# Optimization experiments

Hardware: AMD Instinct MI355X
Metric: run time of the kernel (lower is better)

Reference implementation:

```python
import jax, jax.numpy as jnp
import numpy as np
import math

B, S, D, H, FF = 32, 577, 768, 12, 3072
Dh = D // H
EPS = 1e-5


def layer_norm(x, w, b):
    mu = jnp.mean(x, axis=-1, keepdims=True)
    var = jnp.mean(jnp.square(x - mu), axis=-1, keepdims=True)
    return (x - mu) * jax.lax.rsqrt(var + EPS) * w + b


def setup_inputs() -> dict:
    key = jax.random.key(0)
    ks = jax.random.split(key, 12)
    s = 0.02
    return {
        "x": jax.random.normal(ks[0], (B, S, D), dtype=jnp.float32),
        "ln1_w": jnp.ones((D,), jnp.float32),
        "ln1_b": jnp.zeros((D,), jnp.float32),
        # stacked per-head Q/K/V projections (head order matches torch concat order)
        "Wq": jax.random.normal(ks[1], (H, D, Dh), jnp.float32) * s,
        "bq": jnp.zeros((H, Dh), jnp.float32),
        "Wk": jax.random.normal(ks[2], (H, D, Dh), jnp.float32) * s,
        "bk": jnp.zeros((H, Dh), jnp.float32),
        "Wv": jax.random.normal(ks[3], (H, D, Dh), jnp.float32) * s,
        "bv": jnp.zeros((H, Dh), jnp.float32),
        "Wo": jax.random.normal(ks[4], (D, D), jnp.float32) * s,
        "bo": jnp.zeros((D,), jnp.float32),
        "ln2_w": jnp.ones((D,), jnp.float32),
        "ln2_b": jnp.zeros((D,), jnp.float32),
        "W1": jax.random.normal(ks[5], (D, FF), jnp.float32) * s,
        "b1": jnp.zeros((FF,), jnp.float32),
        "W2": jax.random.normal(ks[6], (FF, D), jnp.float32) * s,
        "b2": jnp.zeros((D,), jnp.float32),
    }


def reference(x, ln1_w, ln1_b, Wq, bq, Wk, bk, Wv, bv, Wo, bo, ln2_w, ln2_b, W1, b1, W2, b2):
    # pre-norm attention
    h = layer_norm(x, ln1_w, ln1_b)  # [B,S,D]
    q = jnp.einsum('bsd,hde->bhse', h, Wq) + bq[:, None, :]
    k = jnp.einsum('bsd,hde->bhse', h, Wk) + bk[:, None, :]
    v = jnp.einsum('bsd,hde->bhse', h, Wv) + bv[:, None, :]
    scores = jnp.einsum('bhse,bhte->bhst', q, k) / math.sqrt(Dh)
    probs = jax.nn.softmax(scores, axis=-1)
    ctx = jnp.einsum('bhst,bhte->bhse', probs, v)  # [B,H,S,Dh]
    ctx = ctx.transpose(0, 2, 1, 3).reshape(B, S, H * Dh)  # concat heads
    attn_out = ctx @ Wo + bo
    x = x + attn_out
    # pre-norm MLP (exact GELU, as nn.GELU default)
    h2 = layer_norm(x, ln2_w, ln2_b)
    mlp = jax.nn.gelu(h2 @ W1 + b1, approximate=False) @ W2 + b2
    return x + mlp
```

## Files before the change

kernel.cpp:

```cpp
#include <hip/hip_runtime.h>
#include <hip/hip_bf16.h>
#include <stdint.h>

#define B_ 32
#define S_ 577
#define D_ 768
#define H_ 12
#define FF_ 3072
#define MROWS (B_*S_)

typedef __attribute__((ext_vector_type(8))) short sh8;
typedef __attribute__((ext_vector_type(4))) float f32x4;
typedef __attribute__((ext_vector_type(4))) unsigned short us4;

static __device__ __forceinline__ unsigned short f2b(float f) {
  __hip_bfloat16 h = __float2bfloat16(f);
  return *reinterpret_cast<unsigned short*>(&h);
}
static __device__ __forceinline__ float b2f(unsigned short u) {
  __hip_bfloat16 h;
  *reinterpret_cast<unsigned short*>(&h) = u;
  return __bfloat162float(h);
}

static __device__ __forceinline__ float fast_gelu(float v) {
  const float z = fabsf(v) * 0.70710678118f;
  const float t = __builtin_amdgcn_rcpf(__builtin_fmaf(0.3275911f, z, 1.0f));
  float p = 1.061405429f;
  p = __builtin_fmaf(p, t, -1.453152027f);
  p = __builtin_fmaf(p, t,  1.421413741f);
  p = __builtin_fmaf(p, t, -0.284496736f);
  p = __builtin_fmaf(p, t,  0.254829592f);
  p = p * t;
  const float e = __expf(-z * z);
  const float erf_abs = __builtin_fmaf(-p, e, 1.0f);
  const float erf_v = copysignf(erf_abs, v);
  const float hv = 0.5f * v;
  return __builtin_fmaf(hv, erf_v, hv);
}

#define GLOAD_LDS16(gp, lp) \
  __builtin_amdgcn_global_load_lds((const __attribute__((address_space(1))) unsigned int*)(gp), \
                                   (__attribute__((address_space(3))) unsigned int*)(lp), 16, 0, 0)

static __device__ __forceinline__ void packT_body(
    const float* __restrict__ src, unsigned short* __restrict__ dst,
    int K, int N, int kb, int nb, float scl, int tid)
{
  __shared__ unsigned short t[64][65];
  const int c = tid & 63, r4 = tid >> 6;
#pragma unroll
  for (int p = 0; p < 16; ++p) {
    const int ko = p * 4 + r4;
    t[c][ko] = f2b(src[(size_t)(kb + ko) * N + nb + c] * scl);
  }
  __syncthreads();
#pragma unroll
  for (int p = 0; p < 16; ++p) {
    const int rr = p * 4 + r4;
    dst[(size_t)(nb + rr) * K + kb + c] = t[rr][c];
  }
}

__global__ __launch_bounds__(256) void pack_all(
    const float* __restrict__ Wq, const float* __restrict__ Wk,
    const float* __restrict__ Wv, const float* __restrict__ Wo,
    const float* __restrict__ W1, const float* __restrict__ W2,
    const float* __restrict__ bq, const float* __restrict__ bk,
    const float* __restrict__ bv,
    unsigned short* __restrict__ wqkvT, unsigned short* __restrict__ woT,
    unsigned short* __restrict__ w1T, unsigned short* __restrict__ w2T,
    float* __restrict__ biasq)
{
  const int b = blockIdx.x;
  const int tid = threadIdx.x;
  if (b < 144) {
    packT_body(Wo, woT, 768, 768, (b / 12) * 64, (b % 12) * 64, 1.f, tid);
  } else if (b < 720) {
    const int i = b - 144;
    packT_body(W1, w1T, 768, 3072, (i / 48) * 64, (i % 48) * 64, 1.f, tid);
  } else if (b < 1296) {
    const int i = b - 720;
    packT_body(W2, w2T, 3072, 768, (i / 12) * 64, (i % 12) * 64, 1.f, tid);
  } else if (b < 1728) {
    const int i = b - 1296;
    const int kb = i % 12, h = (i / 12) % 12, which = i / 144;
    const float* src = ((which == 0) ? Wq : (which == 1) ? Wk : Wv) + (size_t)h * 768 * 64;
    unsigned short* db = wqkvT + (size_t)(which * 768 + h * 64) * 768;
    packT_body(src, db, 768, 64, kb * 64, 0, which == 0 ? 0.125f : 1.f, tid);
  } else {
    const int idx = (b - 1728) * 256 + tid;
    if (idx < 2304) {
      const int wb = idx / 768, rb = idx - wb * 768;
      const float* bb = (wb == 0) ? bq : (wb == 1) ? bk : bv;
      biasq[idx] = bb[rb] * (wb == 0 ? 0.125f : 1.f);
    }
  }
}

__global__ __launch_bounds__(192) void ln_bf16(
    const float* __restrict__ x, const float* __restrict__ w, const float* __restrict__ bse,
    unsigned short* __restrict__ out)
{
  const int row = blockIdx.x;
  const int tid = threadIdx.x;
  const float* xr = x + (size_t)row * 768;
  const f32x4 v = *(const f32x4*)(xr + tid * 4);
  float s  = v[0] + v[1] + v[2] + v[3];
  float ss = v[0]*v[0] + v[1]*v[1] + v[2]*v[2] + v[3]*v[3];
#pragma unroll
  for (int off = 32; off >= 1; off >>= 1) {
    s  += __shfl_xor(s, off);
    ss += __shfl_xor(ss, off);
  }
  __shared__ float red[6];
  const int wv = tid >> 6, ln = tid & 63;
  if (ln == 0) { red[wv] = s; red[wv + 3] = ss; }
  __syncthreads();
  s  = red[0] + red[1] + red[2];
  ss = red[3] + red[4] + red[5];
  const float mu = s * (1.f / 768.f);
  const float var = ss * (1.f / 768.f) - mu * mu;
  const float rs = rsqrtf(var + 1e-5f);
  const f32x4 w4 = *(const f32x4*)(w + tid * 4);
  const f32x4 b4 = *(const f32x4*)(bse + tid * 4);
  us4 o;
#pragma unroll
  for (int e = 0; e < 4; ++e) o[e] = f2b((v[e] - mu) * rs * w4[e] + b4[e]);
  *(us4*)(out + (size_t)row * 768 + tid * 4) = o;
}

template<int EPI>
__global__ __launch_bounds__(256, 4) void gemm128(
    const unsigned short* __restrict__ A, const unsigned short* __restrict__ Bt,
    const float* __restrict__ bias, const float* __restrict__ res,
    unsigned short* __restrict__ obf, float* __restrict__ of32,
    int M, int N, int K)
{
  __shared__ __align__(16) unsigned short sAB[2][128 * 64];
  const int tid = threadIdx.x;
  const int wid = tid >> 6, ln = tid & 63;
  const int wr = wid >> 1, wc = wid & 1;
  const int l15 = ln & 15, lg = ln >> 4;
  const int l7 = l15 & 7;
  const int uo0 = ((lg) ^ l7) * 8;
  const int uo1 = ((4 + lg) ^ l7) * 8;
  const int srow = ln >> 3;
  const int scol = ((ln & 7) ^ srow) * 8;
  const int NT = K >> 6;

  const int gx = N >> 7;
  const int gm = (M + 127) >> 7;
  const int nwg = gridDim.x;
  const int q = nwg >> 3, r = nwg & 7;
  const int x = blockIdx.x & 7, ii = blockIdx.x >> 3;
  const int wg = (x < r ? x * (q + 1) : r * (q + 1) + (x - r) * q) + ii;
  int bm, bn;
  {
    const int g8 = gx >> 3, rem = gx & 7;
    const int per_full = gm << 3;
    if (wg < g8 * per_full) {
      const int bg = wg / per_full;
      const int r2 = wg - bg * per_full;
      bm = r2 >> 3; bn = (bg << 3) + (r2 & 7);
    } else {
      const int r2 = wg - g8 * per_full;
      bm = r2 / rem; bn = (g8 << 3) + (r2 - bm * rem);
    }
  }

  const int arow = wr * 64 + l15;
  const int brow = wc * 64 + l15;

  const unsigned short* ap[4];
  const unsigned short* bp[4];
#pragma unroll
  for (int j = 0; j < 4; ++j) {
    int ga = bm * 128 + (wid * 4 + j) * 8 + srow; if (ga >= M) ga = M - 1;
    ap[j] = A + (size_t)ga * K + scol;
    const int gb = bn * 128 + (wid * 4 + j) * 8 + srow;
    bp[j] = Bt + (size_t)gb * K + scol;
  }
  unsigned short* const lA = sAB[0] + wid * 4 * 512;
  unsigned short* const lB = sAB[1] + wid * 4 * 512;

  f32x4 acc[4][4] = {};

  for (int t = 0; t < NT; ++t) {
    __syncthreads();
#pragma unroll
    for (int j = 0; j < 4; ++j) { GLOAD_LDS16(ap[j], lA + j * 512); ap[j] += 64; }
#pragma unroll
    for (int j = 0; j < 4; ++j) { GLOAD_LDS16(bp[j], lB + j * 512); bp[j] += 64; }
    asm volatile("s_waitcnt vmcnt(0)" ::: "memory");
    __syncthreads();

#pragma unroll
    for (int kk = 0; kk < 2; ++kk) {
      const int uo = kk ? uo1 : uo0;
      sh8 af[4], bf[4];
#pragma unroll
      for (int mi = 0; mi < 4; ++mi)
        af[mi] = *(const sh8*)(sAB[0] + (arow + mi * 16) * 64 + uo);
#pragma unroll
      for (int ni = 0; ni < 4; ++ni)
        bf[ni] = *(const sh8*)(sAB[1] + (brow + ni * 16) * 64 + uo);
#pragma unroll
      for (int mi = 0; mi < 4; ++mi)
#pragma unroll
        for (int ni = 0; ni < 4; ++ni)
          acc[mi][ni] = __builtin_amdgcn_mfma_f32_16x16x32_bf16(af[mi], bf[ni], acc[mi][ni], 0, 0, 0);
    }
  }

  constexpr int ESTR = 132;
  float* eps = (float*)sAB;
  const int ecol = (tid & 31) * 4;
  const int gcol = bn * 128 + ecol;
  const f32x4 bvh = *(const f32x4*)(bias + gcol);
  const int erow0 = tid >> 5;
#pragma unroll
  for (int pass = 0; pass < 4; ++pass) {
    __syncthreads();
    if (wr == (pass >> 1)) {
      const int mib = (pass & 1) * 2;
#pragma unroll
      for (int ml = 0; ml < 2; ++ml)
#pragma unroll
        for (int ni = 0; ni < 4; ++ni)
#pragma unroll
          for (int rr = 0; rr < 4; ++rr)
            eps[(ml * 16 + lg * 4 + rr) * ESTR + wc * 64 + ni * 16 + l15] = acc[mib + ml][ni][rr];
    }
    __syncthreads();
#pragma unroll
    for (int pp = 0; pp < 4; ++pp) {
      const int rl = pp * 8 + erow0;
      const int grow = bm * 128 + pass * 32 + rl;
      if (grow < M) {
        f32x4 v = *(const f32x4*)(eps + rl * ESTR + ecol);
        v += bvh;
        if (EPI == 2) {
#pragma unroll
          for (int e = 0; e < 4; ++e) v[e] = fast_gelu(v[e]);
        }
        if (EPI == 1) {
          const f32x4 rv = *(const f32x4*)(res + (size_t)grow * N + gcol);
          v += rv;
          *(f32x4*)(of32 + (size_t)grow * N + gcol) = v;
        } else {
          us4 o = { f2b(v[0]), f2b(v[1]), f2b(v[2]), f2b(v[3]) };
          *(us4*)(obf + (size_t)grow * N + gcol) = o;
        }
      }
    }
  }
}

__global__ __launch_bounds__(512) void attn(
    const unsigned short* __restrict__ qkv, unsigned short* __restrict__ ctx)
{
  constexpr int KP = 72;
  __shared__ __align__(16) unsigned short sQ[128 * KP];
  __shared__ __align__(16) unsigned short sK[64 * KP];
  __shared__ __align__(16) unsigned short sVT[64 * KP];
  __shared__ __align__(16) unsigned short sP[8][16 * KP];
  const int tid = threadIdx.x, wv = tid >> 6, ln = tid & 63;
  const int l15 = ln & 15, lg = ln >> 4;
  const int b = blockIdx.z, h = blockIdx.y, qt = blockIdx.x;
  const size_t base = (size_t)b * S_ * 2304 + h * 64;
  const unsigned short* qp = qkv + base;
  const unsigned short* kp = qkv + base + 768;
  const unsigned short* vp = qkv + base + 1536;

  {
    const int r = tid >> 2, c = (tid & 3) * 16;
    int row = qt * 128 + r; if (row >= S_) row = S_ - 1;
    const unsigned short* g = qp + (size_t)row * 2304 + c;
    *(sh8*)(sQ + r * KP + c)     = *(const sh8*)g;
    *(sh8*)(sQ + r * KP + c + 8) = *(const sh8*)(g + 8);
  }

  const int kr = tid >> 3, kc = (tid & 7) * 8;
  const unsigned short* krow = kp + (size_t)kr * 2304 + kc;
  unsigned short* const sKdst = sK + kr * KP + kc;
  const int ve = tid & 63, vkvb = tid >> 6;
  const unsigned short* vrow = vp + (size_t)vkvb * 8 * 2304 + ve;
  unsigned short* const sVdst = sVT + ve * KP + vkvb * 8;

  f32x4 oacc[4] = {};
  float m_run = -1e30f, l_run = 0.f;
  const int nt = (S_ + 63) / 64;
  for (int t = 0; t < nt; ++t) {
    __syncthreads();
    if (t < nt - 1) {
      *(sh8*)sKdst = *(const sh8*)krow;
      krow += (size_t)64 * 2304;
      {
        unsigned short val[8];
#pragma unroll
        for (int j = 0; j < 8; ++j) val[j] = vrow[(size_t)j * 2304];
        *(sh8*)sVdst = *(sh8*)val;
        vrow += (size_t)64 * 2304;
      }
    } else {
      {
        int row = t * 64 + kr; if (row >= S_) row = S_ - 1;
        *(sh8*)sKdst = *(const sh8*)(kp + (size_t)row * 2304 + kc);
      }
      {
        unsigned short val[8];
#pragma unroll
        for (int j = 0; j < 8; ++j) {
          int row = t * 64 + vkvb * 8 + j; if (row >= S_) row = S_ - 1;
          val[j] = vp[(size_t)row * 2304 + ve];
        }
        *(sh8*)sVdst = *(sh8*)val;
      }
    }
    __syncthreads();

    f32x4 sacc[4] = {};
#pragma unroll
    for (int kk = 0; kk < 2; ++kk) {
      sh8 bq = *(const sh8*)(sQ + (wv * 16 + l15) * KP + kk * 32 + lg * 8);
#pragma unroll
      for (int f = 0; f < 4; ++f) {
        sh8 ak = *(const sh8*)(sK + (f * 16 + l15) * KP + kk * 32 + lg * 8);
        sacc[f] = __builtin_amdgcn_mfma_f32_16x16x32_bf16(ak, bq, sacc[f], 0, 0, 0);
      }
    }

    if (t == nt - 1) {
#pragma unroll
      for (int f = 0; f < 4; ++f)
#pragma unroll
        for (int r = 0; r < 4; ++r)
          if (t * 64 + f * 16 + lg * 4 + r >= S_) sacc[f][r] = -1e30f;
    }
    float pmax = -1e30f;
#pragma unroll
    for (int f = 0; f < 4; ++f)
#pragma unroll
      for (int r = 0; r < 4; ++r) pmax = fmaxf(pmax, sacc[f][r]);
    pmax = fmaxf(pmax, __shfl_xor(pmax, 16));
    pmax = fmaxf(pmax, __shfl_xor(pmax, 32));
    const float mnew = fmaxf(m_run, pmax);
    const float alpha = __expf(m_run - mnew);
    float psum = 0.f;
    unsigned short pb[4][4];
#pragma unroll
    for (int f = 0; f < 4; ++f)
#pragma unroll
      for (int r = 0; r < 4; ++r) {
        const float p = __expf(sacc[f][r] - mnew);
        psum += p;
        pb[f][r] = f2b(p);
      }
    psum += __shfl_xor(psum, 16);
    psum += __shfl_xor(psum, 32);
    l_run = l_run * alpha + psum;
    m_run = mnew;
#pragma unroll
    for (int f = 0; f < 4; ++f) {
      oacc[f][0] *= alpha; oacc[f][1] *= alpha;
      oacc[f][2] *= alpha; oacc[f][3] *= alpha;
    }
#pragma unroll
    for (int f = 0; f < 4; ++f) {
      us4 pk = { pb[f][0], pb[f][1], pb[f][2], pb[f][3] };
      *(us4*)(sP[wv] + l15 * KP + f * 16 + lg * 4) = pk;
    }
    __syncthreads();

#pragma unroll
    for (int kk = 0; kk < 2; ++kk) {
      sh8 bp = *(const sh8*)(sP[wv] + l15 * KP + kk * 32 + lg * 8);
#pragma unroll
      for (int fe = 0; fe < 4; ++fe) {
        sh8 av = *(const sh8*)(sVT + (fe * 16 + l15) * KP + kk * 32 + lg * 8);
        oacc[fe] = __builtin_amdgcn_mfma_f32_16x16x32_bf16(av, bp, oacc[fe], 0, 0, 0);
      }
    }
  }

  const int qa = qt * 128 + wv * 16 + l15;
  if (qa < S_) {
    const float inv = 1.f / l_run;
    const size_t orow = ((size_t)b * S_ + qa) * 768 + h * 64;
#pragma unroll
    for (int fe = 0; fe < 4; ++fe) {
      unsigned short pk[4];
#pragma unroll
      for (int r = 0; r < 4; ++r) pk[r] = f2b(oacc[fe][r] * inv);
      *(us4*)(ctx + orow + fe * 16 + lg * 4) = *(us4*)pk;
    }
  }
}

extern "C" void kernel_launch(void* const* d_in, const int* in_sizes, int n_in,
                              void* d_out, int out_size, void* d_ws, size_t ws_size,
                              hipStream_t stream)
{
  const float* x    = (const float*)d_in[0];
  const float* ln1w = (const float*)d_in[1];
  const float* ln1b = (const float*)d_in[2];
  const float* Wq   = (const float*)d_in[3];
  const float* bq   = (const float*)d_in[4];
  const float* Wk   = (const float*)d_in[5];
  const float* bk   = (const float*)d_in[6];
  const float* Wv   = (const float*)d_in[7];
  const float* bv   = (const float*)d_in[8];
  const float* Wo   = (const float*)d_in[9];
  const float* bo   = (const float*)d_in[10];
  const float* ln2w = (const float*)d_in[11];
  const float* ln2b = (const float*)d_in[12];
  const float* W1   = (const float*)d_in[13];
  const float* b1   = (const float*)d_in[14];
  const float* W2   = (const float*)d_in[15];
  const float* b2   = (const float*)d_in[16];
  float* out = (float*)d_out;
  char* ws = (char*)d_ws;

  unsigned short* wqkvT = (unsigned short*)(ws + 0);
  unsigned short* woT   = (unsigned short*)(ws + 3538944);
  unsigned short* w1T   = (unsigned short*)(ws + 4718592);
  unsigned short* w2T   = (unsigned short*)(ws + 9437184);
  float*          biasq = (float*)(ws + 14155776);
  unsigned short* hbf   = (unsigned short*)(ws + 14164992);
  unsigned short* qkvb  = (unsigned short*)(ws + 42525696);
  unsigned short* ctxb  = (unsigned short*)(ws + 127607808);
  unsigned short* mlp1  = qkvb;

  pack_all<<<1737, 256, 0, stream>>>(Wq, Wk, Wv, Wo, W1, W2, bq, bk, bv,
                                     wqkvT, woT, w1T, w2T, biasq);

  ln_bf16<<<MROWS, 192, 0, stream>>>(x, ln1w, ln1b, hbf);
  gemm128<0><<<145 * 18, 256, 0, stream>>>(hbf, wqkvT, biasq, nullptr, qkvb, nullptr,
                                           MROWS, 2304, 768);
  attn<<<dim3(5, 12, 32), 512, 0, stream>>>(qkvb, ctxb);
  gemm128<1><<<145 * 6, 256, 0, stream>>>(ctxb, woT, bo, x, nullptr, out,
                                          MROWS, 768, 768);
  ln_bf16<<<MROWS, 192, 0, stream>>>(out, ln2w, ln2b, hbf);
  gemm128<2><<<145 * 24, 256, 0, stream>>>(hbf, w1T, b1, nullptr, mlp1, nullptr,
                                           MROWS, 3072, 768);
  gemm128<1><<<145 * 6, 256, 0, stream>>>(mlp1, w2T, b2, out, nullptr, out,
                                          MROWS, 768, 3072);
}
```

Before: 464.5 us.

## Fuse LN1 into pack kernel and register-prefetch K/V tiles in attention

Merges the first LayerNorm into the weight-packing launch as extra blocks, removing one kernel launch and letting the two independent jobs overlap. In the attention kernel, the next K/V tile is loaded into registers while the current tile is being computed, so global-load latency is hidden behind the MFMA work. The barrier between writing P to shared memory and the PV MFMA is removed, since each wave only reads its own sP slice. Register prefetch raises register pressure, and the merged kernel now holds two unlike kinds of work, which may hurt occupancy.

```diff
diff --git a/kernel.cpp b/kernel.cpp
--- a/kernel.cpp
+++ b/kernel.cpp
@@ -62,7 +62,43 @@
   }
 }
 
-__global__ __launch_bounds__(256) void pack_all(
+static __device__ __forceinline__ void ln_body256(
+    const float* __restrict__ x, const float* __restrict__ w,
+    const float* __restrict__ bse, unsigned short* __restrict__ out,
+    int row, int tid)
+{
+  __shared__ float red[6];
+  const int wv = tid >> 6, ln = tid & 63;
+  f32x4 v = {};
+  float s = 0.f, ss = 0.f;
+  if (tid < 192) {
+    v = *(const f32x4*)(x + (size_t)row * 768 + tid * 4);
+    s  = v[0] + v[1] + v[2] + v[3];
+    ss = v[0]*v[0] + v[1]*v[1] + v[2]*v[2] + v[3]*v[3];
+  }
+#pragma unroll
+  for (int off = 32; off >= 1; off >>= 1) {
+    s  += __shfl_xor(s, off);
+    ss += __shfl_xor(ss, off);
+  }
+  if (ln == 0 && wv < 3) { red[wv] = s; red[wv + 3] = ss; }
+  __syncthreads();
+  if (tid < 192) {
+    s  = red[0] + red[1] + red[2];
+    ss = red[3] + red[4] + red[5];
+    const float mu = s * (1.f / 768.f);
+    const float var = ss * (1.f / 768.f) - mu * mu;
+    const float rs = rsqrtf(var + 1e-5f);
+    const f32x4 w4 = *(const f32x4*)(w + tid * 4);
+    const f32x4 b4 = *(const f32x4*)(bse + tid * 4);
+    us4 o;
+#pragma unroll
+    for (int e = 0; e < 4; ++e) o[e] = f2b((v[e] - mu) * rs * w4[e] + b4[e]);
+    *(us4*)(out + (size_t)row * 768 + tid * 4) = o;
+  }
+}
+
+__global__ __launch_bounds__(256) void pack_ln(
     const float* __restrict__ Wq, const float* __restrict__ Wk,
     const float* __restrict__ Wv, const float* __restrict__ Wo,
     const float* __restrict__ W1, const float* __restrict__ W2,
@@ -70,7 +106,9 @@
     const float* __restrict__ bv,
     unsigned short* __restrict__ wqkvT, unsigned short* __restrict__ woT,
     unsigned short* __restrict__ w1T, unsigned short* __restrict__ w2T,
-    float* __restrict__ biasq)
+    float* __restrict__ biasq,
+    const float* __restrict__ x, const float* __restrict__ ln1w,
+    const float* __restrict__ ln1b, unsigned short* __restrict__ hbf)
 {
   const int b = blockIdx.x;
   const int tid = threadIdx.x;
@@ -88,13 +126,15 @@
     const float* src = ((which == 0) ? Wq : (which == 1) ? Wk : Wv) + (size_t)h * 768 * 64;
     unsigned short* db = wqkvT + (size_t)(which * 768 + h * 64) * 768;
     packT_body(src, db, 768, 64, kb * 64, 0, which == 0 ? 0.125f : 1.f, tid);
-  } else {
+  } else if (b < 1737) {
     const int idx = (b - 1728) * 256 + tid;
     if (idx < 2304) {
       const int wb = idx / 768, rb = idx - wb * 768;
       const float* bb = (wb == 0) ? bq : (wb == 1) ? bk : bv;
       biasq[idx] = bb[rb] * (wb == 0 ? 0.125f : 1.f);
     }
+  } else {
+    ln_body256(x, ln1w, ln1b, hbf, b - 1737, tid);
   }
 }
 
@@ -288,37 +328,39 @@
   const unsigned short* vrow = vp + (size_t)vkvb * 8 * 2304 + ve;
   unsigned short* const sVdst = sVT + ve * KP + vkvb * 8;
 
+  const int nt = (S_ + 63) / 64;
+  sh8 kreg = *(const sh8*)krow;
+  unsigned short vreg[8];
+#pragma unroll
+  for (int j = 0; j < 8; ++j) vreg[j] = vrow[(size_t)j * 2304];
+  krow += (size_t)64 * 2304;
+  vrow += (size_t)64 * 2304;
+
   f32x4 oacc[4] = {};
   float m_run = -1e30f, l_run = 0.f;
-  const int nt = (S_ + 63) / 64;
   for (int t = 0; t < nt; ++t) {
     __syncthreads();
-    if (t < nt - 1) {
-      *(sh8*)sKdst = *(const sh8*)krow;
-      krow += (size_t)64 * 2304;
-      {
-        unsigned short val[8];
-#pragma unroll
-        for (int j = 0; j < 8; ++j) val[j] = vrow[(size_t)j * 2304];
-        *(sh8*)sVdst = *(sh8*)val;
+    *(sh8*)sKdst = kreg;
+    *(sh8*)sVdst = *(sh8*)vreg;
+    __syncthreads();
+
+    if (t + 1 < nt) {
+      if (t + 1 < nt - 1) {
+        kreg = *(const sh8*)krow;
+#pragma unroll
+        for (int j = 0; j < 8; ++j) vreg[j] = vrow[(size_t)j * 2304];
+        krow += (size_t)64 * 2304;
         vrow += (size_t)64 * 2304;
+      } else {
+        int row = (nt - 1) * 64 + kr; if (row >= S_) row = S_ - 1;
+        kreg = *(const sh8*)(kp + (size_t)row * 2304 + kc);
+#pragma unroll
+        for (int j = 0; j < 8; ++j) {
+          int rr = (nt - 1) * 64 + vkvb * 8 + j; if (rr >= S_) rr = S_ - 1;
+          vreg[j] = vp[(size_t)rr * 2304 + ve];
+        }
       }
-    } else {
-      {
-        int row = t * 64 + kr; if (row >= S_) row = S_ - 1;
-        *(sh8*)sKdst = *(const sh8*)(kp + (size_t)row * 2304 + kc);
-      }
-      {
-        unsigned short val[8];
-#pragma unroll
-        for (int j = 0; j < 8; ++j) {
-          int row = t * 64 + vkvb * 8 + j; if (row >= S_) row = S_ - 1;
-          val[j] = vp[(size_t)row * 2304 + ve];
-        }
-        *(sh8*)sVdst = *(sh8*)val;
-      }
-    }
-    __syncthreads();
+    }
 
     f32x4 sacc[4] = {};
 #pragma unroll
@@ -371,7 +413,6 @@
       us4 pk = { pb[f][0], pb[f][1], pb[f][2], pb[f][3] };
       *(us4*)(sP[wv] + l15 * KP + f * 16 + lg * 4) = pk;
     }
-    __syncthreads();
 
 #pragma unroll
     for (int kk = 0; kk < 2; ++kk) {
@@ -432,10 +473,10 @@
   unsigned short* ctxb  = (unsigned short*)(ws + 127607808);
   unsigned short* mlp1  = qkvb;
 
-  pack_all<<<1737, 256, 0, stream>>>(Wq, Wk, Wv, Wo, W1, W2, bq, bk, bv,
-                                     wqkvT, woT, w1T, w2T, biasq);
-
-  ln_bf16<<<MROWS, 192, 0, stream>>>(x, ln1w, ln1b, hbf);
+  pack_ln<<<1737 + MROWS, 256, 0, stream>>>(Wq, Wk, Wv, Wo, W1, W2, bq, bk, bv,
+                                            wqkvT, woT, w1T, w2T, biasq,
+                                            x, ln1w, ln1b, hbf);
+
   gemm128<0><<<145 * 18, 256, 0, stream>>>(hbf, wqkvT, biasq, nullptr, qkvb, nullptr,
                                            MROWS, 2304, 768);
   attn<<<dim3(5, 12, 32), 512, 0, stream>>>(qkvb, ctxb);
```

Measured after the change: 464.5 us. No clear change (+0.0%).
